# Optimization experiments

Measured on AMD Instinct MI355X. Metric: run time of the kernel, lower is better.

The kernel has to match this reference:

```python
import jax, jax.numpy as jnp
import numpy as np

B, D, T, R = 8, 128, 32768, 2
C = D // R  # reduced channel dim = 64


def conv1x1(x, w, b):
    # x: [B, Cin, T], w: [Cout, Cin], b: [Cout] -> [B, Cout, T]
    return jnp.einsum('oi,bit->bot', w, x) + b[None, :, None]


def setup_inputs() -> dict:
    key = jax.random.key(0)
    ks = jax.random.split(key, 16)
    inp = {
        'x1': jax.random.normal(ks[0], (B, D, T), dtype=jnp.float32),
        'x2': jnp.zeros((B, D, T), dtype=jnp.float32),  # unused in encoder stage
        'mask': jnp.ones((B, 1, T), dtype=jnp.float32),
        # 1x1 conv projections (weights squeezed to [out, in])
        'wq': jax.random.normal(ks[1], (C, D), dtype=jnp.float32) * 0.05,
        'bq': jnp.zeros((C,), dtype=jnp.float32),
        'wk': jax.random.normal(ks[2], (C, D), dtype=jnp.float32) * 0.05,
        'bk': jnp.zeros((C,), dtype=jnp.float32),
        'wv': jax.random.normal(ks[3], (C, D), dtype=jnp.float32) * 0.05,
        'bv': jnp.zeros((C,), dtype=jnp.float32),
        # E, F: Linear(C -> C) with bias
        'we': jax.random.normal(ks[4], (C, C), dtype=jnp.float32) * 0.1,
        'be': jnp.zeros((C,), dtype=jnp.float32),
        'wf': jax.random.normal(ks[5], (C, C), dtype=jnp.float32) * 0.1,
        'bf': jnp.zeros((C,), dtype=jnp.float32),
        # output 1x1 conv: C -> D
        'wo': jax.random.normal(ks[6], (D, C), dtype=jnp.float32) * 0.05,
        'bo': jnp.zeros((D,), dtype=jnp.float32),
    }
    return inp


def reference(x1, x2, mask, wq, bq, wk, bk, wv, bv, we, be, wf, bf, wo, bo):
    # Q/K/V projections (encoder stage: value from x1; x2 unused)
    Q = conv1x1(x1, wq, bq)              # [B, C, T]
    K = conv1x1(x1, wk, bk)              # [B, C, T]
    V = conv1x1(x1, wv, bv)              # [B, C, T]
    # K = E(K^T): [B, T, C] @ we^T + be
    Kp = jnp.einsum('bct,oc->bto', K, we) + be  # [B, T, C]
    # S = Q @ Kp -> [B, C, C], scaled by sqrt(last dim)
    S = jnp.einsum('bct,btk->bck', Q, Kp)
    P = jax.nn.softmax(S / jnp.sqrt(jnp.asarray(S.shape[-1], S.dtype)), axis=-1)
    # dropout is identity in eval mode
    # V = (F(V^T))^T: [B, C, T]
    Vp = jnp.einsum('bct,oc->bot', V, wf) + bf[None, :, None]  # [B, C, T]
    out = jnp.einsum('bck,bkt->bct', P, Vp)  # [B, C, T]
    out = conv1x1(jax.nn.relu(out), wo, bo)  # [B, D, T]
    return out * mask[:, 0:1, :]
```

## Files before the change

### kernel.cpp

```cpp
#include <hip/hip_runtime.h>
#include <stdint.h>
#include <stddef.h>

#define B_ 8
#define D_ 128
#define T_ 32768
#define C_ 64
#define NCHUNK 32

typedef __bf16 bf16;
typedef __bf16 bf16x8 __attribute__((ext_vector_type(8)));
typedef float f32x4 __attribute__((ext_vector_type(4)));
typedef float f32x16 __attribute__((ext_vector_type(16)));

__device__ __forceinline__ f32x16 zero16() {
  f32x16 z;
#pragma unroll
  for (int i = 0; i < 16; ++i) z[i] = 0.f;
  return z;
}
__device__ __forceinline__ bf16x8 cvt8(f32x4 lo, f32x4 hi) {
  bf16x8 r;
#pragma unroll
  for (int j = 0; j < 4; ++j) { r[j] = (bf16)lo[j]; r[j + 4] = (bf16)hi[j]; }
  return r;
}

__global__ __launch_bounds__(256) void k0_zero(float* __restrict__ p, int n)
{
  int i = blockIdx.x * 256 + threadIdx.x;
  if (i < n) p[i] = 0.f;
}

__global__ __launch_bounds__(256) void k1_gram(
    const float* __restrict__ x1,
    const float* __restrict__ we, const float* __restrict__ wk,
    const float* __restrict__ bk, const float* __restrict__ be,
    const float* __restrict__ wf, const float* __restrict__ wv,
    const float* __restrict__ bv, const float* __restrict__ bfv,
    float* __restrict__ G, float* __restrict__ r,
    float* __restrict__ wkp, float* __restrict__ wvp,
    float* __restrict__ bkp, float* __restrict__ bvp)
{
  const int blk = blockIdx.x;
  const int tid = threadIdx.x;
  const int ngram = B_ * NCHUNK;

  if (blk >= ngram) {
    const int wb = blk - ngram;
    const float* wa  = (wb < 32) ? we : wf;
    const float* wb2 = (wb < 32) ? wk : wv;
    float* outw      = (wb < 32) ? wkp : wvp;
    const int idx = (wb & 31) * 256 + tid;
    const int o = idx >> 7, d = idx & 127;
    float s = 0.f;
    for (int c = 0; c < 64; ++c) s += wa[o * 64 + c] * wb2[c * 128 + d];
    outw[idx] = s;
    if (tid < 64) {
      if (wb == 0) {
        float t = 0.f;
        for (int c = 0; c < 64; ++c) t += we[tid * 64 + c] * bk[c];
        bkp[tid] = t + be[tid];
      } else if (wb == 32) {
        float t = 0.f;
        for (int c = 0; c < 64; ++c) t += wf[tid * 64 + c] * bv[c];
        bvp[tid] = t + bfv[tid];
      }
    }
    return;
  }

  const int b  = blk / NCHUNK;
  const int ch = blk % NCHUNK;
  const int Tc = T_ / NCHUNK;
  const int t0 = ch * Tc;
  const int wave = tid >> 6, lane = tid & 63;
  const int lrow = lane & 31, lk = lane >> 5;
  const int qa = wave >> 1, qb = wave & 1;

  const float* xb = x1 + (size_t)b * D_ * T_;
  const float* pa0 = xb + (size_t)(64 * qa + lrow) * T_ + 8 * lk;
  const float* pa1 = pa0 + (size_t)32 * T_;
  const float* pb0 = xb + (size_t)(64 * qb + lrow) * T_ + 8 * lk;
  const float* pb1 = pb0 + (size_t)32 * T_;

  f32x16 acc00 = zero16(), acc01 = zero16(), acc10 = zero16(), acc11 = zero16();
  float rsum = 0.f;

  for (int t = t0; t < t0 + Tc; t += 16) {
    f32x4 a0l = *(const f32x4*)(pa0 + t), a0h = *(const f32x4*)(pa0 + t + 4);
    f32x4 a1l = *(const f32x4*)(pa1 + t), a1h = *(const f32x4*)(pa1 + t + 4);
    f32x4 b0l = *(const f32x4*)(pb0 + t), b0h = *(const f32x4*)(pb0 + t + 4);
    f32x4 b1l = *(const f32x4*)(pb1 + t), b1h = *(const f32x4*)(pb1 + t + 4);
    bf16x8 fa0 = cvt8(a0l, a0h);
    bf16x8 fa1 = cvt8(a1l, a1h);
    bf16x8 fb0 = cvt8(b0l, b0h);
    bf16x8 fb1 = cvt8(b1l, b1h);
    f32x4 ol = qb ? a1l : a0l, oh = qb ? a1h : a0h;
#pragma unroll
    for (int j = 0; j < 4; ++j) rsum += ol[j] + oh[j];
    acc00 = __builtin_amdgcn_mfma_f32_32x32x16_bf16(fa0, fb0, acc00, 0, 0, 0);
    acc01 = __builtin_amdgcn_mfma_f32_32x32x16_bf16(fa0, fb1, acc01, 0, 0, 0);
    acc10 = __builtin_amdgcn_mfma_f32_32x32x16_bf16(fa1, fb0, acc10, 0, 0, 0);
    acc11 = __builtin_amdgcn_mfma_f32_32x32x16_bf16(fa1, fb1, acc11, 0, 0, 0);
  }

  float* gb = G + (size_t)b * 16384;
#pragma unroll
  for (int rr = 0; rr < 16; ++rr) {
    const int rloc = (rr & 3) + 8 * (rr >> 2) + 4 * lk;
    const int r0 = 64 * qa + rloc, r1 = 64 * qa + 32 + rloc;
    const int c0 = 64 * qb + lrow, c1 = 64 * qb + 32 + lrow;
    atomicAdd(&gb[r0 * 128 + c0], acc00[rr]);
    atomicAdd(&gb[r0 * 128 + c1], acc01[rr]);
    atomicAdd(&gb[r1 * 128 + c0], acc10[rr]);
    atomicAdd(&gb[r1 * 128 + c1], acc11[rr]);
  }
  float rtot = rsum + __shfl_xor(rsum, 32, 64);
  if (lk == 0) atomicAdd(&r[b * 128 + 32 * wave + lrow], rtot);
}

__global__ __launch_bounds__(128) void k3_softmax(
    const float* __restrict__ wq, const float* __restrict__ bq,
    const float* __restrict__ G, const float* __restrict__ r,
    const float* __restrict__ wkp, const float* __restrict__ wvp,
    const float* __restrict__ bkp, const float* __restrict__ bvp,
    bf16* __restrict__ attw, float* __restrict__ attb)
{
  const int b = blockIdx.x >> 6, c = blockIdx.x & 63;
  const int tid = threadIdx.x;
  __shared__ float sM[128], sR[128], sQ[128], sP[64];
  __shared__ float sRed;

  const float* Gb = G + (size_t)b * 16384;
  const float* wqc = wq + c * 128;

  const float rv = r[b * 128 + tid];
  sR[tid] = rv;
  float m = 0.f;
  for (int j = 0; j < 128; ++j) m += wqc[j] * Gb[j * 128 + tid];
  sM[tid] = m;
  sQ[tid] = wqc[tid] * rv;
  __syncthreads();

  if (tid < 64) {
    float q2 = sQ[tid] + sQ[tid + 64];
#pragma unroll
    for (int off = 32; off; off >>= 1) q2 += __shfl_xor(q2, off, 64);
    if (tid == 0) sRed = q2;
  }
  __syncthreads();
  const float qr = sRed;
  const float bqc = bq[c];

  if (tid < 64) {
    const int k = tid;
    float s = 0.f, wkr = 0.f;
    for (int i = 0; i < 128; ++i) {
      const float w = wkp[k * 128 + i];
      s += sM[i] * w;
      wkr += sR[i] * w;
    }
    const float bk2 = bkp[k];
    float logit = (s + bqc * wkr + bk2 * qr + (float)T_ * bqc * bk2) * 0.125f;
    float mx = logit;
#pragma unroll
    for (int off = 32; off; off >>= 1) mx = fmaxf(mx, __shfl_xor(mx, off, 64));
    const float e = __expf(logit - mx);
    float sum = e;
#pragma unroll
    for (int off = 32; off; off >>= 1) sum += __shfl_xor(sum, off, 64);
    sP[k] = e / sum;
  }
  __syncthreads();

  {
    float aw = 0.f;
    for (int k = 0; k < 64; ++k) aw += sP[k] * wvp[k * 128 + tid];
    attw[((size_t)b * 64 + c) * 128 + tid] = (bf16)aw;
  }
  if (tid < 64) {
    float pb = sP[tid] * bvp[tid];
#pragma unroll
    for (int off = 32; off; off >>= 1) pb += __shfl_xor(pb, off, 64);
    if (tid == 0) attb[b * 64 + c] = pb;
  }
}

__global__ __launch_bounds__(256) void k4_out(
    const float* __restrict__ x1, const float* __restrict__ mask,
    const float* __restrict__ wo, const float* __restrict__ bo,
    const bf16* __restrict__ attw, const float* __restrict__ attb,
    float* __restrict__ out)
{
  __shared__ bf16 x_lds[128 * 128];
  __shared__ bf16 m1_lds[64 * 128];
  __shared__ float bo_lds[128];
  __shared__ float ab_lds[64];

  const int b = blockIdx.x >> 8;
  const int t0 = (blockIdx.x & 255) * 128;
  const int tid = threadIdx.x;
  const int wave = tid >> 6, lane = tid & 63;
  const int lrow = lane & 31, lk = lane >> 5;
  const float* xb = x1 + (size_t)b * D_ * T_;

  {
    const int dr = tid >> 4;
    const int tc = (tid & 15) * 8;
#pragma unroll
    for (int it = 0; it < 8; ++it) {
      const int d = it * 16 + dr;
      f32x4 lo = *(const f32x4*)(xb + (size_t)d * T_ + t0 + tc);
      f32x4 hi = *(const f32x4*)(xb + (size_t)d * T_ + t0 + tc + 4);
      *(bf16x8*)&x_lds[d * 128 + tc] = cvt8(lo, hi);
    }
  }
  if (tid < 128) bo_lds[tid] = bo[tid];
  if (tid < 64) ab_lds[tid] = attb[b * 64 + tid];
  __syncthreads();

  const int tcol = 32 * wave + lrow;

  f32x16 p0 = zero16(), p1 = zero16();
  const bf16* awb = attw + (size_t)b * 64 * 128;
#pragma unroll
  for (int k0 = 0; k0 < 128; k0 += 16) {
    bf16x8 a0 = *(const bf16x8*)(awb + (size_t)(lrow) * 128 + k0 + 8 * lk);
    bf16x8 a1 = *(const bf16x8*)(awb + (size_t)(32 + lrow) * 128 + k0 + 8 * lk);
    bf16x8 bx;
#pragma unroll
    for (int j = 0; j < 8; ++j) bx[j] = x_lds[(k0 + 8 * lk + j) * 128 + tcol];
    p0 = __builtin_amdgcn_mfma_f32_32x32x16_bf16(a0, bx, p0, 0, 0, 0);
    p1 = __builtin_amdgcn_mfma_f32_32x32x16_bf16(a1, bx, p1, 0, 0, 0);
  }
#pragma unroll
  for (int rr = 0; rr < 16; ++rr) {
    const int row = (rr & 3) + 8 * (rr >> 2) + 4 * lk;
    m1_lds[row * 128 + tcol]        = (bf16)fmaxf(p0[rr] + ab_lds[row], 0.f);
    m1_lds[(32 + row) * 128 + tcol] = (bf16)fmaxf(p1[rr] + ab_lds[32 + row], 0.f);
  }
  __syncthreads();

  f32x16 q0 = zero16(), q1 = zero16(), q2 = zero16(), q3 = zero16();
#pragma unroll
  for (int k0 = 0; k0 < 64; k0 += 16) {
    bf16x8 bm;
#pragma unroll
    for (int j = 0; j < 8; ++j) bm[j] = m1_lds[(k0 + 8 * lk + j) * 128 + tcol];
#pragma unroll
    for (int i = 0; i < 4; ++i) {
      const float* wrow = wo + (size_t)(32 * i + lrow) * 64 + k0 + 8 * lk;
      bf16x8 wfrag = cvt8(*(const f32x4*)wrow, *(const f32x4*)(wrow + 4));
      if (i == 0) q0 = __builtin_amdgcn_mfma_f32_32x32x16_bf16(wfrag, bm, q0, 0, 0, 0);
      if (i == 1) q1 = __builtin_amdgcn_mfma_f32_32x32x16_bf16(wfrag, bm, q1, 0, 0, 0);
      if (i == 2) q2 = __builtin_amdgcn_mfma_f32_32x32x16_bf16(wfrag, bm, q2, 0, 0, 0);
      if (i == 3) q3 = __builtin_amdgcn_mfma_f32_32x32x16_bf16(wfrag, bm, q3, 0, 0, 0);
    }
  }

  const float mv = mask[(size_t)b * T_ + t0 + tcol];
  float* ob = out + (size_t)b * D_ * T_ + t0 + tcol;
#pragma unroll
  for (int rr = 0; rr < 16; ++rr) {
    const int row = (rr & 3) + 8 * (rr >> 2) + 4 * lk;
    ob[(size_t)(row) * T_]      = (q0[rr] + bo_lds[row]) * mv;
    ob[(size_t)(32 + row) * T_] = (q1[rr] + bo_lds[32 + row]) * mv;
    ob[(size_t)(64 + row) * T_] = (q2[rr] + bo_lds[64 + row]) * mv;
    ob[(size_t)(96 + row) * T_] = (q3[rr] + bo_lds[96 + row]) * mv;
  }
}

extern "C" void kernel_launch(void* const* d_in, const int* in_sizes, int n_in,
                              void* d_out, int out_size, void* d_ws, size_t ws_size,
                              hipStream_t stream)
{
  const float* x1   = (const float*)d_in[0];
  const float* mask = (const float*)d_in[2];
  const float* wq   = (const float*)d_in[3];
  const float* bq   = (const float*)d_in[4];
  const float* wk   = (const float*)d_in[5];
  const float* bk   = (const float*)d_in[6];
  const float* wv   = (const float*)d_in[7];
  const float* bv   = (const float*)d_in[8];
  const float* we   = (const float*)d_in[9];
  const float* be   = (const float*)d_in[10];
  const float* wf   = (const float*)d_in[11];
  const float* bfv  = (const float*)d_in[12];
  const float* wo   = (const float*)d_in[13];
  const float* bo   = (const float*)d_in[14];
  float* out = (float*)d_out;

  float* G   = (float*)d_ws;
  float* r   = G + (size_t)B_ * 16384;
  float* wkp = r + B_ * 128;
  float* wvp = wkp + 8192;
  float* bkp = wvp + 8192;
  float* bvp = bkp + 64;
  float* attb = bvp + 64;
  bf16*  attw = (bf16*)(attb + B_ * 64);

  const int nzero = B_ * 16384 + B_ * 128;
  k0_zero<<<(nzero + 255) / 256, 256, 0, stream>>>(G, nzero);
  k1_gram<<<B_ * NCHUNK + 64, 256, 0, stream>>>(x1, we, wk, bk, be, wf, wv, bv, bfv,
                                                G, r, wkp, wvp, bkp, bvp);
  k3_softmax<<<B_ * 64, 128, 0, stream>>>(wq, bq, G, r, wkp, wvp, bkp, bvp, attw, attb);
  k4_out<<<B_ * (T_ / 128), 256, 0, stream>>>(x1, mask, wo, bo, attw, attb, out);
}
```

Baseline: 425.1 us.

## Stage Gram tiles through LDS, raise chunk count, pre-convert wo to bf16

The Gram kernel now splits T into 128 chunks per batch instead of 32, giving more blocks. Each block loads 64-column tiles of x1 into padded LDS as bf16, so every element is read from global memory once instead of by multiple waves. The output kernel drops its x1 LDS staging and reads x1 straight from global per column. It stores the intermediate transposed in a padded per-thread row without a barrier and uses a bf16 copy of wo produced by extra blocks in the Gram kernel. The changes add syncs and many more atomics into G, and the output kernel's strided scalar global loads may coalesce poorly.

Result: faster. 416.1 us (-2.1%).

```diff
diff --git a/kernel.cpp b/kernel.cpp
--- a/kernel.cpp
+++ b/kernel.cpp
@@ -6,9 +6,10 @@
 #define D_ 128
 #define T_ 32768
 #define C_ 64
-#define NCHUNK 32
+#define NCH_ 128
 
 typedef __bf16 bf16;
+typedef __bf16 bf16x4 __attribute__((ext_vector_type(4)));
 typedef __bf16 bf16x8 __attribute__((ext_vector_type(8)));
 typedef float f32x4 __attribute__((ext_vector_type(4)));
 typedef float f32x16 __attribute__((ext_vector_type(16)));
@@ -19,12 +20,6 @@
   for (int i = 0; i < 16; ++i) z[i] = 0.f;
   return z;
 }
-__device__ __forceinline__ bf16x8 cvt8(f32x4 lo, f32x4 hi) {
-  bf16x8 r;
-#pragma unroll
-  for (int j = 0; j < 4; ++j) { r[j] = (bf16)lo[j]; r[j + 4] = (bf16)hi[j]; }
-  return r;
-}
 
 __global__ __launch_bounds__(256) void k0_zero(float* __restrict__ p, int n)
 {
@@ -32,77 +27,100 @@
   if (i < n) p[i] = 0.f;
 }
 
-__global__ __launch_bounds__(256) void k1_gram(
+__global__ __launch_bounds__(256, 4) void k1_gram(
     const float* __restrict__ x1,
     const float* __restrict__ we, const float* __restrict__ wk,
     const float* __restrict__ bk, const float* __restrict__ be,
     const float* __restrict__ wf, const float* __restrict__ wv,
     const float* __restrict__ bv, const float* __restrict__ bfv,
+    const float* __restrict__ wo,
     float* __restrict__ G, float* __restrict__ r,
     float* __restrict__ wkp, float* __restrict__ wvp,
-    float* __restrict__ bkp, float* __restrict__ bvp)
+    float* __restrict__ bkp, float* __restrict__ bvp,
+    bf16* __restrict__ wobf)
 {
   const int blk = blockIdx.x;
   const int tid = threadIdx.x;
-  const int ngram = B_ * NCHUNK;
+  const int ngram = B_ * NCH_;
 
   if (blk >= ngram) {
     const int wb = blk - ngram;
-    const float* wa  = (wb < 32) ? we : wf;
-    const float* wb2 = (wb < 32) ? wk : wv;
-    float* outw      = (wb < 32) ? wkp : wvp;
-    const int idx = (wb & 31) * 256 + tid;
-    const int o = idx >> 7, d = idx & 127;
-    float s = 0.f;
-    for (int c = 0; c < 64; ++c) s += wa[o * 64 + c] * wb2[c * 128 + d];
-    outw[idx] = s;
-    if (tid < 64) {
-      if (wb == 0) {
-        float t = 0.f;
-        for (int c = 0; c < 64; ++c) t += we[tid * 64 + c] * bk[c];
-        bkp[tid] = t + be[tid];
-      } else if (wb == 32) {
-        float t = 0.f;
-        for (int c = 0; c < 64; ++c) t += wf[tid * 64 + c] * bv[c];
-        bvp[tid] = t + bfv[tid];
+    if (wb < 64) {
+      const float* wa  = (wb < 32) ? we : wf;
+      const float* wb2 = (wb < 32) ? wk : wv;
+      float* outw      = (wb < 32) ? wkp : wvp;
+      const int idx = (wb & 31) * 256 + tid;
+      const int o = idx >> 7, d = idx & 127;
+      float s = 0.f;
+      for (int c = 0; c < 64; ++c) s += wa[o * 64 + c] * wb2[c * 128 + d];
+      outw[idx] = s;
+      if (tid < 64) {
+        if (wb == 0) {
+          float t = 0.f;
+          for (int c = 0; c < 64; ++c) t += we[tid * 64 + c] * bk[c];
+          bkp[tid] = t + be[tid];
+        } else if (wb == 32) {
+          float t = 0.f;
+          for (int c = 0; c < 64; ++c) t += wf[tid * 64 + c] * bv[c];
+          bvp[tid] = t + bfv[tid];
+        }
       }
+    } else {
+      const int idx = (wb - 64) * 256 + tid;
+      wobf[idx] = (bf16)wo[idx];
     }
     return;
   }
 
-  const int b  = blk / NCHUNK;
-  const int ch = blk % NCHUNK;
-  const int Tc = T_ / NCHUNK;
-  const int t0 = ch * Tc;
+  __shared__ bf16 x_s[128 * 72];
+
+  const int b  = blk >> 7;
+  const int ch = blk & (NCH_ - 1);
+  const int t0 = ch * (T_ / NCH_);
   const int wave = tid >> 6, lane = tid & 63;
   const int lrow = lane & 31, lk = lane >> 5;
   const int qa = wave >> 1, qb = wave & 1;
 
   const float* xb = x1 + (size_t)b * D_ * T_;
-  const float* pa0 = xb + (size_t)(64 * qa + lrow) * T_ + 8 * lk;
-  const float* pa1 = pa0 + (size_t)32 * T_;
-  const float* pb0 = xb + (size_t)(64 * qb + lrow) * T_ + 8 * lk;
-  const float* pb1 = pb0 + (size_t)32 * T_;
 
   f32x16 acc00 = zero16(), acc01 = zero16(), acc10 = zero16(), acc11 = zero16();
   float rsum = 0.f;
 
-  for (int t = t0; t < t0 + Tc; t += 16) {
-    f32x4 a0l = *(const f32x4*)(pa0 + t), a0h = *(const f32x4*)(pa0 + t + 4);
-    f32x4 a1l = *(const f32x4*)(pa1 + t), a1h = *(const f32x4*)(pa1 + t + 4);
-    f32x4 b0l = *(const f32x4*)(pb0 + t), b0h = *(const f32x4*)(pb0 + t + 4);
-    f32x4 b1l = *(const f32x4*)(pb1 + t), b1h = *(const f32x4*)(pb1 + t + 4);
-    bf16x8 fa0 = cvt8(a0l, a0h);
-    bf16x8 fa1 = cvt8(a1l, a1h);
-    bf16x8 fb0 = cvt8(b0l, b0h);
-    bf16x8 fb1 = cvt8(b1l, b1h);
-    f32x4 ol = qb ? a1l : a0l, oh = qb ? a1h : a0h;
-#pragma unroll
-    for (int j = 0; j < 4; ++j) rsum += ol[j] + oh[j];
-    acc00 = __builtin_amdgcn_mfma_f32_32x32x16_bf16(fa0, fb0, acc00, 0, 0, 0);
-    acc01 = __builtin_amdgcn_mfma_f32_32x32x16_bf16(fa0, fb1, acc01, 0, 0, 0);
-    acc10 = __builtin_amdgcn_mfma_f32_32x32x16_bf16(fa1, fb0, acc10, 0, 0, 0);
-    acc11 = __builtin_amdgcn_mfma_f32_32x32x16_bf16(fa1, fb1, acc11, 0, 0, 0);
+  const int scol = (tid & 15) * 4;
+  const int srow0 = tid >> 4;
+
+  const bf16* A0  = &x_s[(64 * qa + lrow) * 72 + 8 * lk];
+  const bf16* A1  = A0 + 32 * 72;
+  const bf16* Bb0 = &x_s[(64 * qb + lrow) * 72 + 8 * lk];
+  const bf16* Bb1 = Bb0 + 32 * 72;
+
+  for (int s = 0; s < 4; ++s) {
+    const int tb = t0 + s * 64;
+    if (s) __syncthreads();
+#pragma unroll
+    for (int it = 0; it < 8; ++it) {
+      const int row = it * 16 + srow0;
+      f32x4 v = *(const f32x4*)(xb + (size_t)row * T_ + tb + scol);
+      bf16x4 h;
+#pragma unroll
+      for (int j = 0; j < 4; ++j) h[j] = (bf16)v[j];
+      *(bf16x4*)&x_s[row * 72 + scol] = h;
+    }
+    __syncthreads();
+#pragma unroll
+    for (int k = 0; k < 4; ++k) {
+      bf16x8 fa0 = *(const bf16x8*)(A0 + 16 * k);
+      bf16x8 fa1 = *(const bf16x8*)(A1 + 16 * k);
+      bf16x8 fb0 = *(const bf16x8*)(Bb0 + 16 * k);
+      bf16x8 fb1 = *(const bf16x8*)(Bb1 + 16 * k);
+      bf16x8 own = qb ? fa1 : fa0;
+#pragma unroll
+      for (int j = 0; j < 8; ++j) rsum += (float)own[j];
+      acc00 = __builtin_amdgcn_mfma_f32_32x32x16_bf16(fa0, fb0, acc00, 0, 0, 0);
+      acc01 = __builtin_amdgcn_mfma_f32_32x32x16_bf16(fa0, fb1, acc01, 0, 0, 0);
+      acc10 = __builtin_amdgcn_mfma_f32_32x32x16_bf16(fa1, fb0, acc10, 0, 0, 0);
+      acc11 = __builtin_amdgcn_mfma_f32_32x32x16_bf16(fa1, fb1, acc11, 0, 0, 0);
+    }
   }
 
   float* gb = G + (size_t)b * 16384;
@@ -187,76 +205,62 @@
   }
 }
 
-__global__ __launch_bounds__(256) void k4_out(
+__global__ __launch_bounds__(256, 4) void k4_out(
     const float* __restrict__ x1, const float* __restrict__ mask,
-    const float* __restrict__ wo, const float* __restrict__ bo,
+    const bf16* __restrict__ wobf, const float* __restrict__ bo,
     const bf16* __restrict__ attw, const float* __restrict__ attb,
     float* __restrict__ out)
 {
-  __shared__ bf16 x_lds[128 * 128];
-  __shared__ bf16 m1_lds[64 * 128];
-  __shared__ float bo_lds[128];
-  __shared__ float ab_lds[64];
+  __shared__ bf16 m1[128 * 72];
+  __shared__ float bo_s[128];
+  __shared__ float ab_s[64];
 
   const int b = blockIdx.x >> 8;
-  const int t0 = (blockIdx.x & 255) * 128;
+  const int t0 = (blockIdx.x & 255) << 7;
   const int tid = threadIdx.x;
   const int wave = tid >> 6, lane = tid & 63;
   const int lrow = lane & 31, lk = lane >> 5;
-  const float* xb = x1 + (size_t)b * D_ * T_;
-
-  {
-    const int dr = tid >> 4;
-    const int tc = (tid & 15) * 8;
-#pragma unroll
-    for (int it = 0; it < 8; ++it) {
-      const int d = it * 16 + dr;
-      f32x4 lo = *(const f32x4*)(xb + (size_t)d * T_ + t0 + tc);
-      f32x4 hi = *(const f32x4*)(xb + (size_t)d * T_ + t0 + tc + 4);
-      *(bf16x8*)&x_lds[d * 128 + tc] = cvt8(lo, hi);
-    }
-  }
-  if (tid < 128) bo_lds[tid] = bo[tid];
-  if (tid < 64) ab_lds[tid] = attb[b * 64 + tid];
+  const int tcol = 32 * wave + lrow;
+
+  if (tid < 128) bo_s[tid] = bo[tid];
+  if (tid < 64) ab_s[tid] = attb[b * 64 + tid];
   __syncthreads();
 
-  const int tcol = 32 * wave + lrow;
+  const float* xc = x1 + (size_t)b * D_ * T_ + t0 + tcol;
+  const bf16* awb = attw + (size_t)b * 8192;
 
   f32x16 p0 = zero16(), p1 = zero16();
-  const bf16* awb = attw + (size_t)b * 64 * 128;
-#pragma unroll
-  for (int k0 = 0; k0 < 128; k0 += 16) {
-    bf16x8 a0 = *(const bf16x8*)(awb + (size_t)(lrow) * 128 + k0 + 8 * lk);
-    bf16x8 a1 = *(const bf16x8*)(awb + (size_t)(32 + lrow) * 128 + k0 + 8 * lk);
+#pragma unroll
+  for (int k0 = 0; k0 < 8; ++k0) {
+    bf16x8 a0 = *(const bf16x8*)(awb + (size_t)lrow * 128 + 16 * k0 + 8 * lk);
+    bf16x8 a1 = *(const bf16x8*)(awb + (size_t)(32 + lrow) * 128 + 16 * k0 + 8 * lk);
     bf16x8 bx;
 #pragma unroll
-    for (int j = 0; j < 8; ++j) bx[j] = x_lds[(k0 + 8 * lk + j) * 128 + tcol];
+    for (int j = 0; j < 8; ++j)
+      bx[j] = (bf16)xc[(size_t)(16 * k0 + 8 * lk + j) * T_];
     p0 = __builtin_amdgcn_mfma_f32_32x32x16_bf16(a0, bx, p0, 0, 0, 0);
     p1 = __builtin_amdgcn_mfma_f32_32x32x16_bf16(a1, bx, p1, 0, 0, 0);
   }
+  bf16* mrow = &m1[tcol * 72];
 #pragma unroll
   for (int rr = 0; rr < 16; ++rr) {
     const int row = (rr & 3) + 8 * (rr >> 2) + 4 * lk;
-    m1_lds[row * 128 + tcol]        = (bf16)fmaxf(p0[rr] + ab_lds[row], 0.f);
-    m1_lds[(32 + row) * 128 + tcol] = (bf16)fmaxf(p1[rr] + ab_lds[32 + row], 0.f);
-  }
-  __syncthreads();
+    mrow[row]      = (bf16)fmaxf(p0[rr] + ab_s[row], 0.f);
+    mrow[32 + row] = (bf16)fmaxf(p1[rr] + ab_s[32 + row], 0.f);
+  }
 
   f32x16 q0 = zero16(), q1 = zero16(), q2 = zero16(), q3 = zero16();
 #pragma unroll
-  for (int k0 = 0; k0 < 64; k0 += 16) {
-    bf16x8 bm;
-#pragma unroll
-    for (int j = 0; j < 8; ++j) bm[j] = m1_lds[(k0 + 8 * lk + j) * 128 + tcol];
-#pragma unroll
-    for (int i = 0; i < 4; ++i) {
-      const float* wrow = wo + (size_t)(32 * i + lrow) * 64 + k0 + 8 * lk;
-      bf16x8 wfrag = cvt8(*(const f32x4*)wrow, *(const f32x4*)(wrow + 4));
-      if (i == 0) q0 = __builtin_amdgcn_mfma_f32_32x32x16_bf16(wfrag, bm, q0, 0, 0, 0);
-      if (i == 1) q1 = __builtin_amdgcn_mfma_f32_32x32x16_bf16(wfrag, bm, q1, 0, 0, 0);
-      if (i == 2) q2 = __builtin_amdgcn_mfma_f32_32x32x16_bf16(wfrag, bm, q2, 0, 0, 0);
-      if (i == 3) q3 = __builtin_amdgcn_mfma_f32_32x32x16_bf16(wfrag, bm, q3, 0, 0, 0);
-    }
+  for (int k0 = 0; k0 < 4; ++k0) {
+    bf16x8 bm = *(const bf16x8*)(mrow + 16 * k0 + 8 * lk);
+    bf16x8 w0 = *(const bf16x8*)(wobf + (size_t)(lrow) * 64 + 16 * k0 + 8 * lk);
+    bf16x8 w1 = *(const bf16x8*)(wobf + (size_t)(32 + lrow) * 64 + 16 * k0 + 8 * lk);
+    bf16x8 w2 = *(const bf16x8*)(wobf + (size_t)(64 + lrow) * 64 + 16 * k0 + 8 * lk);
+    bf16x8 w3 = *(const bf16x8*)(wobf + (size_t)(96 + lrow) * 64 + 16 * k0 + 8 * lk);
+    q0 = __builtin_amdgcn_mfma_f32_32x32x16_bf16(w0, bm, q0, 0, 0, 0);
+    q1 = __builtin_amdgcn_mfma_f32_32x32x16_bf16(w1, bm, q1, 0, 0, 0);
+    q2 = __builtin_amdgcn_mfma_f32_32x32x16_bf16(w2, bm, q2, 0, 0, 0);
+    q3 = __builtin_amdgcn_mfma_f32_32x32x16_bf16(w3, bm, q3, 0, 0, 0);
   }
 
   const float mv = mask[(size_t)b * T_ + t0 + tcol];
@@ -264,10 +268,10 @@
 #pragma unroll
   for (int rr = 0; rr < 16; ++rr) {
     const int row = (rr & 3) + 8 * (rr >> 2) + 4 * lk;
-    ob[(size_t)(row) * T_]      = (q0[rr] + bo_lds[row]) * mv;
-    ob[(size_t)(32 + row) * T_] = (q1[rr] + bo_lds[32 + row]) * mv;
-    ob[(size_t)(64 + row) * T_] = (q2[rr] + bo_lds[64 + row]) * mv;
-    ob[(size_t)(96 + row) * T_] = (q3[rr] + bo_lds[96 + row]) * mv;
+    ob[(size_t)(row) * T_]      = (q0[rr] + bo_s[row]) * mv;
+    ob[(size_t)(32 + row) * T_] = (q1[rr] + bo_s[32 + row]) * mv;
+    ob[(size_t)(64 + row) * T_] = (q2[rr] + bo_s[64 + row]) * mv;
+    ob[(size_t)(96 + row) * T_] = (q3[rr] + bo_s[96 + row]) * mv;
   }
 }
 
@@ -291,19 +295,23 @@
   const float* bo   = (const float*)d_in[14];
   float* out = (float*)d_out;
 
-  float* G   = (float*)d_ws;
-  float* r   = G + (size_t)B_ * 16384;
-  float* wkp = r + B_ * 128;
-  float* wvp = wkp + 8192;
-  float* bkp = wvp + 8192;
-  float* bvp = bkp + 64;
-  float* attb = bvp + 64;
-  bf16*  attw = (bf16*)(attb + B_ * 64);
+  char* base = (char*)d_ws;
+  size_t off = 0;
+  float* G    = (float*)(base + off); off += (size_t)B_ * 16384 * 4;
+  float* r    = (float*)(base + off); off += (size_t)B_ * 128 * 4;
+  float* wkp  = (float*)(base + off); off += 8192 * 4;
+  float* wvp  = (float*)(base + off); off += 8192 * 4;
+  float* bkp  = (float*)(base + off); off += 64 * 4;
+  float* bvp  = (float*)(base + off); off += 64 * 4;
+  float* attb = (float*)(base + off); off += (size_t)B_ * 64 * 4;
+  bf16* attw  = (bf16*)(base + off);  off += (size_t)B_ * 64 * 128 * 2;
+  bf16* wobf  = (bf16*)(base + off);  off += 8192 * 2;
 
   const int nzero = B_ * 16384 + B_ * 128;
   k0_zero<<<(nzero + 255) / 256, 256, 0, stream>>>(G, nzero);
-  k1_gram<<<B_ * NCHUNK + 64, 256, 0, stream>>>(x1, we, wk, bk, be, wf, wv, bv, bfv,
-                                                G, r, wkp, wvp, bkp, bvp);
+  k1_gram<<<B_ * NCH_ + 96, 256, 0, stream>>>(
+      x1, we, wk, bk, be, wf, wv, bv, bfv, wo,
+      G, r, wkp, wvp, bkp, bvp, wobf);
   k3_softmax<<<B_ * 64, 128, 0, stream>>>(wq, bq, G, r, wkp, wvp, bkp, bvp, attw, attb);
-  k4_out<<<B_ * (T_ / 128), 256, 0, stream>>>(x1, mask, wo, bo, attw, attb, out);
-}
+  k4_out<<<B_ * (T_ / 128), 256, 0, stream>>>(x1, mask, wobf, bo, attw, attb, out);
+}
```
